# Kernel optimization log

Hardware: AMD Instinct MI355X
Metric: run time of the kernel (lower is better)

## Reference

```python
import jax, jax.numpy as jnp
import numpy as np

N_NODES = 100000
N_EDGES = 1600000
EMBED = 64


def setup_inputs() -> dict:
    key = jax.random.key(0)
    ks = jax.random.split(key, 8)
    scale = 1.0 / np.sqrt(EMBED)
    return {
        "embeddings": jax.random.normal(ks[0], (N_NODES, EMBED), dtype=jnp.float32),
        "edge_index": jax.random.randint(ks[1], (2, N_EDGES), 0, N_NODES, dtype=jnp.int32),
        "W1": jax.random.normal(ks[2], (EMBED, EMBED), dtype=jnp.float32) * scale,
        "b1": jnp.zeros((EMBED,), dtype=jnp.float32),
        "W2": jax.random.normal(ks[3], (EMBED, EMBED), dtype=jnp.float32) * scale,
        "b2": jnp.zeros((EMBED,), dtype=jnp.float32),
        "W3": jax.random.normal(ks[4], (EMBED, EMBED), dtype=jnp.float32) * scale,
        "b3": jnp.zeros((EMBED,), dtype=jnp.float32),
    }


def _gcn_layer(x, W, b, src, dst, n):
    # PyG GCNConv: add self-loops, symmetric normalization D^-1/2 (A+I) D^-1/2, then XW + b.
    x = x @ W  # [N, H]
    # degree from destination column, including the self-loop (+1)
    deg = jnp.zeros((n,), dtype=x.dtype).at[dst].add(1.0) + 1.0
    dinv = jax.lax.rsqrt(deg)  # deg >= 1, safe
    norm = dinv[src] * dinv[dst]  # [E]
    msg = x[src] * norm[:, None]  # [E, H] gather + scale
    out = jax.ops.segment_sum(msg, dst, num_segments=n)  # scatter-add
    out = out + x * (dinv * dinv)[:, None]  # self-loop term
    return out + b


def reference(embeddings, edge_index, W1, b1, W2, b2, W3, b3):
    src, dst = edge_index[0], edge_index[1]
    n = embeddings.shape[0]
    x = _gcn_layer(embeddings, W1, b1, src, dst, n)
    x = _gcn_layer(x, W2, b2, src, dst, n)
    x = _gcn_layer(x, W3, b3, src, dst, n)
    return x
```

## Files before the change

kernel.cpp:

```cpp
#include <hip/hip_runtime.h>

#define N_NODES 100000
#define N_EDGES 1600000
#define NTILES (N_NODES / 16)

#define BKT_SHIFT 8
#define BKT_NODES 256
#define NBK ((N_NODES + BKT_NODES - 1) / BKT_NODES)
#define CHUNK 4096
#define NCHUNKS ((N_EDGES + CHUNK - 1) / CHUNK)
#define BSTRIDE 5120

typedef _Float16 half8 __attribute__((ext_vector_type(8)));
typedef float floatx4 __attribute__((ext_vector_type(4)));

__device__ inline float h2f(unsigned short u) {
    return (float)__builtin_bit_cast(_Float16, u);
}
__device__ inline unsigned short f2h(float f) {
    return __builtin_bit_cast(unsigned short, (_Float16)f);
}

__global__ __launch_bounds__(512) void histA_kernel(const int* __restrict__ dst,
                                                    int* __restrict__ hist2d) {
    __shared__ int hist[NBK];
    int t = threadIdx.x;
    int e0 = blockIdx.x * CHUNK;
    int n = N_EDGES - e0; if (n > CHUNK) n = CHUNK;
    for (int i = t; i < NBK; i += 512) hist[i] = 0;
    __syncthreads();
    for (int i = t; i < n; i += 512) atomicAdd(&hist[dst[e0 + i] >> BKT_SHIFT], 1);
    __syncthreads();
    for (int i = t; i < NBK; i += 512) hist2d[blockIdx.x * NBK + i] = hist[i];
}

__global__ __launch_bounds__(512) void bscan_kernel(const int* __restrict__ hist2d,
                                                    int* __restrict__ base2d,
                                                    int* __restrict__ btot) {
    __shared__ int ss[512];
    int t = threadIdx.x;
    int b = blockIdx.x;
    int v = (t < NCHUNKS) ? hist2d[t * NBK + b] : 0;
    ss[t] = v;
    __syncthreads();
    for (int off = 1; off < 512; off <<= 1) {
        int u = (t >= off) ? ss[t - off] : 0;
        __syncthreads();
        ss[t] += u;
        __syncthreads();
    }
    if (t < NCHUNKS) base2d[t * NBK + b] = ss[t] - v;
    if (t == 511) btot[b] = ss[511];
}

__global__ __launch_bounds__(512) void binA3_kernel(const int* __restrict__ src,
                                                    const int* __restrict__ dst,
                                                    const int* __restrict__ base2d,
                                                    int* __restrict__ csr_tmp) {
    __shared__ int staged[CHUNK];
    __shared__ int delta[CHUNK];
    __shared__ int hist[NBK];
    __shared__ int lcur[NBK];
    __shared__ int gdel[NBK];
    __shared__ int scan_s[512];
    int t = threadIdx.x;
    int e0 = blockIdx.x * CHUNK;
    int n = N_EDGES - e0; if (n > CHUNK) n = CHUNK;

    for (int i = t; i < NBK; i += 512) hist[i] = 0;
    __syncthreads();
    for (int i = t; i < n; i += 512) atomicAdd(&hist[dst[e0 + i] >> BKT_SHIFT], 1);
    __syncthreads();
    int v = (t < NBK) ? hist[t] : 0;
    scan_s[t] = v;
    __syncthreads();
    for (int off = 1; off < 512; off <<= 1) {
        int u = (t >= off) ? scan_s[t - off] : 0;
        __syncthreads();
        scan_s[t] += u;
        __syncthreads();
    }
    if (t < NBK) {
        int excl = scan_s[t] - v;
        lcur[t] = excl;
        gdel[t] = t * BSTRIDE + base2d[blockIdx.x * NBK + t] - excl;
    }
    __syncthreads();
    for (int i = t; i < n; i += 512) {
        int s = src[e0 + i];
        int d = dst[e0 + i];
        int bkt = d >> BKT_SHIFT;
        int slot = atomicAdd(&lcur[bkt], 1);
        staged[slot] = ((d & 255) << 24) | s;
        delta[slot] = gdel[bkt];
    }
    __syncthreads();
    for (int p = t; p < n; p += 512) csr_tmp[delta[p] + p] = staged[p];
}

__global__ __launch_bounds__(512) void binB2_kernel(const int* __restrict__ btot,
                                                    const int* __restrict__ csr_tmp,
                                                    const float* __restrict__ emb,
                                                    int4* __restrict__ nodeinfo,
                                                    float* __restrict__ dinv,
                                                    int* __restrict__ csr,
                                                    unsigned short* __restrict__ Xs) {
    __shared__ int src_s[BSTRIDE];
    __shared__ unsigned char dloc[BSTRIDE];
    __shared__ int out_s[BSTRIDE];
    __shared__ int lcnt[BKT_NODES];
    __shared__ int ss[512];
    __shared__ int lcur[BKT_NODES];
    __shared__ float dinv_s[BKT_NODES];
    int t = threadIdx.x;
    int node0 = blockIdx.x * BKT_NODES;
    int base = blockIdx.x * BSTRIDE;
    int cnt = btot[blockIdx.x];
    if (cnt > BSTRIDE) cnt = BSTRIDE;
    if (t < BKT_NODES) lcnt[t] = 0;
    __syncthreads();
    for (int i = t; i < cnt; i += 512) {
        int e = csr_tmp[base + i];
        int dl = (unsigned int)e >> 24;
        src_s[i] = e & 0x00FFFFFF;
        dloc[i] = (unsigned char)dl;
        atomicAdd(&lcnt[dl], 1);
    }
    __syncthreads();
    int v = (t < BKT_NODES) ? lcnt[t] : 0;
    ss[t] = v;
    __syncthreads();
    for (int off = 1; off < 512; off <<= 1) {
        int u = (t >= off) ? ss[t - off] : 0;
        __syncthreads();
        ss[t] += u;
        __syncthreads();
    }
    int excl = ss[t] - v;
    int node = node0 + t;
    if (t < BKT_NODES) {
        lcur[t] = excl;
        if (node < N_NODES) {
            float dv = rsqrtf((float)v + 1.0f);
            nodeinfo[node] = make_int4(base + excl, v, __float_as_int(dv), 0);
            dinv[node] = dv;
            dinv_s[t] = dv;
        }
    }
    __syncthreads();
    for (int i = t; i < cnt; i += 512) {
        int slot = atomicAdd(&lcur[dloc[i]], 1);
        out_s[slot] = src_s[i];
    }
    __syncthreads();
    for (int i = t; i < cnt; i += 512) csr[base + i] = out_s[i];

    int nn = N_NODES - node0; if (nn > BKT_NODES) nn = BKT_NODES;
    const float4* E = (const float4*)emb;
    ushort4* X = (ushort4*)Xs;
    for (int f = t; f < nn * 16; f += 512) {
        int loc = f >> 4;
        float d = dinv_s[loc];
        float4 val = E[(size_t)(node0 + loc) * 16 + (f & 15)];
        ushort4 p;
        p.x = f2h(val.x * d); p.y = f2h(val.y * d);
        p.z = f2h(val.z * d); p.w = f2h(val.w * d);
        X[(size_t)(node0 + loc) * 16 + (f & 15)] = p;
    }
}

__global__ __launch_bounds__(256) void gather_kernel(
    const unsigned short* __restrict__ Xs,
    const int4* __restrict__ nodeinfo, const int* __restrict__ csr,
    unsigned short* __restrict__ Agg, int n_waves) {
    int lane = threadIdx.x & 63;
    int wid = (blockIdx.x * blockDim.x + threadIdx.x) >> 6;
    int sub = lane >> 4;
    int l16 = lane & 15;
    const ushort4* Xv = (const ushort4*)Xs;
    ushort4* Av = (ushort4*)Agg;

    for (int node = wid; node < N_NODES; node += n_waves) {
        int4 ni = nodeinfo[node];
        int beg = ni.x, end = ni.x + ni.y;
        float di = __int_as_float(ni.z);
        float4 acc = make_float4(0.f, 0.f, 0.f, 0.f);
        if (sub == 0) {
            ushort4 o = Xv[(size_t)node * 16 + l16];
            acc.x = h2f(o.x); acc.y = h2f(o.y); acc.z = h2f(o.z); acc.w = h2f(o.w);
        }
        int i = beg + sub;
        int sA0 = (i      < end) ? csr[i]      : 0;
        int sA1 = (i + 4  < end) ? csr[i + 4]  : 0;
        int sB0 = (i + 8  < end) ? csr[i + 8]  : 0;
        int sB1 = (i + 12 < end) ? csr[i + 12] : 0;
        ushort4 rA0 = Xv[(size_t)sA0 * 16 + l16];
        ushort4 rA1 = Xv[(size_t)sA1 * 16 + l16];
        while (i < end) {
            ushort4 rB0 = Xv[(size_t)sB0 * 16 + l16];
            ushort4 rB1 = Xv[(size_t)sB1 * 16 + l16];
            int sC0 = (i + 16 < end) ? csr[i + 16] : 0;
            int sC1 = (i + 20 < end) ? csr[i + 20] : 0;
            float m1 = (i + 4 < end) ? 1.0f : 0.0f;
            acc.x += h2f(rA0.x); acc.y += h2f(rA0.y);
            acc.z += h2f(rA0.z); acc.w += h2f(rA0.w);
            acc.x = fmaf(h2f(rA1.x), m1, acc.x);
            acc.y = fmaf(h2f(rA1.y), m1, acc.y);
            acc.z = fmaf(h2f(rA1.z), m1, acc.z);
            acc.w = fmaf(h2f(rA1.w), m1, acc.w);
            rA0 = rB0; rA1 = rB1;
            sB0 = sC0; sB1 = sC1;
            i += 8;
        }
        acc.x += __shfl_xor(acc.x, 16, 64); acc.y += __shfl_xor(acc.y, 16, 64);
        acc.z += __shfl_xor(acc.z, 16, 64); acc.w += __shfl_xor(acc.w, 16, 64);
        acc.x += __shfl_xor(acc.x, 32, 64); acc.y += __shfl_xor(acc.y, 32, 64);
        acc.z += __shfl_xor(acc.z, 32, 64); acc.w += __shfl_xor(acc.w, 32, 64);
        if (sub == 0) {
            ushort4 p;
            p.x = f2h(acc.x * di); p.y = f2h(acc.y * di);
            p.z = f2h(acc.z * di); p.w = f2h(acc.w * di);
            Av[(size_t)node * 16 + l16] = p;
        }
    }
}

__global__ __launch_bounds__(256) void mlp_mfma_kernel(
    const unsigned short* __restrict__ A, const float* __restrict__ W,
    const float* __restrict__ b, const float* __restrict__ dinv,
    unsigned short* __restrict__ out16, float* __restrict__ out32) {
    __shared__ __attribute__((aligned(16))) _Float16 Wh[4096];
    __shared__ __attribute__((aligned(16))) _Float16 Wl[4096];
    int tid = threadIdx.x;
    for (int u = tid; u < 4096; u += 256) {
        int kk = u >> 6, col = u & 63;
        int tt = col >> 4, mm = col & 15, cc = kk >> 5, gg = (kk >> 3) & 3, jj = kk & 7;
        float w = W[u];
        _Float16 h = (_Float16)w;
        int di = (tt * 2 + cc) * 512 + gg * 128 + mm * 8 + jj;
        Wh[di] = h;
        Wl[di] = (_Float16)(w - (float)h);
    }
    __syncthreads();

    int l = tid & 63;
    int wv = tid >> 6;
    int m = l & 15;
    int g = l >> 4;
    int tile = blockIdx.x * 4 + wv;
    if (tile >= NTILES) return;
    int node0 = tile * 16;
    int row = node0 + m;

    const half8* Ar = (const half8*)(A + (size_t)row * 64);
    half8 ah0 = Ar[g];
    half8 ah1 = Ar[4 + g];

    float bfrag[4];
#pragma unroll
    for (int t = 0; t < 4; t++) bfrag[t] = b[16 * t + m];
    float dv[4];
#pragma unroll
    for (int r = 0; r < 4; r++) dv[r] = dinv[node0 + 4 * g + r];

#pragma unroll
    for (int t = 0; t < 4; t++) {
        half8 bwh0 = *(const half8*)&Wh[(t * 2 + 0) * 512 + g * 128 + m * 8];
        half8 bwl0 = *(const half8*)&Wl[(t * 2 + 0) * 512 + g * 128 + m * 8];
        half8 bwh1 = *(const half8*)&Wh[(t * 2 + 1) * 512 + g * 128 + m * 8];
        half8 bwl1 = *(const half8*)&Wl[(t * 2 + 1) * 512 + g * 128 + m * 8];
        floatx4 d4 = {0.f, 0.f, 0.f, 0.f};
        d4 = __builtin_amdgcn_mfma_f32_16x16x32_f16(ah0, bwh0, d4, 0, 0, 0);
        d4 = __builtin_amdgcn_mfma_f32_16x16x32_f16(ah0, bwl0, d4, 0, 0, 0);
        d4 = __builtin_amdgcn_mfma_f32_16x16x32_f16(ah1, bwh1, d4, 0, 0, 0);
        d4 = __builtin_amdgcn_mfma_f32_16x16x32_f16(ah1, bwl1, d4, 0, 0, 0);
#pragma unroll
        for (int r = 0; r < 4; r++) {
            float v = d4[r] + bfrag[t];
            size_t idx = (size_t)(node0 + 4 * g + r) * 64 + 16 * t + m;
            if (out16) out16[idx] = f2h(v * dv[r]);
            else out32[idx] = v;
        }
    }
}

extern "C" void kernel_launch(void* const* d_in, const int* in_sizes, int n_in,
                              void* d_out, int out_size, void* d_ws, size_t ws_size,
                              hipStream_t stream) {
    const float* emb = (const float*)d_in[0];
    const int* edge  = (const int*)d_in[1];
    const float* W1 = (const float*)d_in[2];
    const float* b1 = (const float*)d_in[3];
    const float* W2 = (const float*)d_in[4];
    const float* b2 = (const float*)d_in[5];
    const float* W3 = (const float*)d_in[6];
    const float* b3 = (const float*)d_in[7];
    float* out = (float*)d_out;

    const int* src = edge;
    const int* dst = edge + N_EDGES;

    char* ws = (char*)d_ws;
    size_t off = 0;
    int* btot = (int*)(ws + off);        off += 2048;
    int* hist2d = (int*)(ws + off);      off += 612352;
    int* base2d = (int*)(ws + off);      off += 612352;
    int4* nodeinfo = (int4*)(ws + off);  off += 1600512;
    float* dinv = (float*)(ws + off);    off += 400128;
    int* csr_tmp = (int*)(ws + off);     off += 8007680;
    int* csr = (int*)(ws + off);         off += 8007680;
    unsigned short* Xa16 = (unsigned short*)(ws + off); off += 12800000;
    unsigned short* Xb16 = (unsigned short*)(ws + off); off += 12800000;
    unsigned short* Agg = (unsigned short*)(ws + off); off += 12800000;

    histA_kernel<<<NCHUNKS, 512, 0, stream>>>(dst, hist2d);
    bscan_kernel<<<NBK, 512, 0, stream>>>(hist2d, base2d, btot);
    binA3_kernel<<<NCHUNKS, 512, 0, stream>>>(src, dst, base2d, csr_tmp);
    binB2_kernel<<<NBK, 512, 0, stream>>>(btot, csr_tmp, emb, nodeinfo, dinv, csr, Xa16);

    const int GBLOCKS = 2048;
    const int n_waves = GBLOCKS * 256 / 64;
    const int MBLOCKS = (NTILES + 3) / 4;

    gather_kernel<<<GBLOCKS, 256, 0, stream>>>(Xa16, nodeinfo, csr, Agg, n_waves);
    mlp_mfma_kernel<<<MBLOCKS, 256, 0, stream>>>(Agg, W1, b1, dinv, Xb16, nullptr);
    gather_kernel<<<GBLOCKS, 256, 0, stream>>>(Xb16, nodeinfo, csr, Agg, n_waves);
    mlp_mfma_kernel<<<MBLOCKS, 256, 0, stream>>>(Agg, W2, b2, dinv, Xa16, nullptr);
    gather_kernel<<<GBLOCKS, 256, 0, stream>>>(Xa16, nodeinfo, csr, Agg, n_waves);
    mlp_mfma_kernel<<<MBLOCKS, 256, 0, stream>>>(Agg, W3, b3, dinv, nullptr, out);
}
```

Before: 267.6 us.

## Fold bucket scan into binning kernels and reuse precomputed chunk histograms

Removes the separate bucket-scan kernel. Each binning block now computes its own per-bucket global base by summing the histograms of all earlier chunks, and reads its local histogram from hist2d instead of recounting dst with shared atomics. binB2 gets its bucket total through a block reduction over the chunk histograms. This saves one launch and one pass over dst, but later blocks do O(NCHUNKS) strided reads of hist2d per bucket, which is redundant work spread across the grid.

```diff
diff --git a/kernel.cpp b/kernel.cpp
--- a/kernel.cpp
+++ b/kernel.cpp
@@ -34,32 +34,12 @@
     for (int i = t; i < NBK; i += 512) hist2d[blockIdx.x * NBK + i] = hist[i];
 }
 
-__global__ __launch_bounds__(512) void bscan_kernel(const int* __restrict__ hist2d,
-                                                    int* __restrict__ base2d,
-                                                    int* __restrict__ btot) {
-    __shared__ int ss[512];
-    int t = threadIdx.x;
-    int b = blockIdx.x;
-    int v = (t < NCHUNKS) ? hist2d[t * NBK + b] : 0;
-    ss[t] = v;
-    __syncthreads();
-    for (int off = 1; off < 512; off <<= 1) {
-        int u = (t >= off) ? ss[t - off] : 0;
-        __syncthreads();
-        ss[t] += u;
-        __syncthreads();
-    }
-    if (t < NCHUNKS) base2d[t * NBK + b] = ss[t] - v;
-    if (t == 511) btot[b] = ss[511];
-}
-
 __global__ __launch_bounds__(512) void binA3_kernel(const int* __restrict__ src,
                                                     const int* __restrict__ dst,
-                                                    const int* __restrict__ base2d,
+                                                    const int* __restrict__ hist2d,
                                                     int* __restrict__ csr_tmp) {
     __shared__ int staged[CHUNK];
     __shared__ int delta[CHUNK];
-    __shared__ int hist[NBK];
     __shared__ int lcur[NBK];
     __shared__ int gdel[NBK];
     __shared__ int scan_s[512];
@@ -67,11 +47,18 @@
     int e0 = blockIdx.x * CHUNK;
     int n = N_EDGES - e0; if (n > CHUNK) n = CHUNK;
 
-    for (int i = t; i < NBK; i += 512) hist[i] = 0;
-    __syncthreads();
-    for (int i = t; i < n; i += 512) atomicAdd(&hist[dst[e0 + i] >> BKT_SHIFT], 1);
-    __syncthreads();
-    int v = (t < NBK) ? hist[t] : 0;
+    int v = (t < NBK) ? hist2d[blockIdx.x * NBK + t] : 0;
+
+    int base_t = 0;
+    if (t < NBK) {
+        int lim = blockIdx.x, cc = 0;
+        for (; cc + 3 < lim; cc += 4) {
+            base_t += hist2d[(cc + 0) * NBK + t] + hist2d[(cc + 1) * NBK + t]
+                    + hist2d[(cc + 2) * NBK + t] + hist2d[(cc + 3) * NBK + t];
+        }
+        for (; cc < lim; cc++) base_t += hist2d[cc * NBK + t];
+    }
+
     scan_s[t] = v;
     __syncthreads();
     for (int off = 1; off < 512; off <<= 1) {
@@ -83,7 +70,7 @@
     if (t < NBK) {
         int excl = scan_s[t] - v;
         lcur[t] = excl;
-        gdel[t] = t * BSTRIDE + base2d[blockIdx.x * NBK + t] - excl;
+        gdel[t] = t * BSTRIDE + base_t - excl;
     }
     __syncthreads();
     for (int i = t; i < n; i += 512) {
@@ -98,7 +85,7 @@
     for (int p = t; p < n; p += 512) csr_tmp[delta[p] + p] = staged[p];
 }
 
-__global__ __launch_bounds__(512) void binB2_kernel(const int* __restrict__ btot,
+__global__ __launch_bounds__(512) void binB2_kernel(const int* __restrict__ hist2d,
                                                     const int* __restrict__ csr_tmp,
                                                     const float* __restrict__ emb,
                                                     int4* __restrict__ nodeinfo,
@@ -115,8 +102,19 @@
     int t = threadIdx.x;
     int node0 = blockIdx.x * BKT_NODES;
     int base = blockIdx.x * BSTRIDE;
-    int cnt = btot[blockIdx.x];
+
+    int part = 0;
+    for (int cc = t; cc < NCHUNKS; cc += 512) part += hist2d[cc * NBK + blockIdx.x];
+    ss[t] = part;
+    __syncthreads();
+    for (int off = 256; off > 0; off >>= 1) {
+        if (t < off) ss[t] += ss[t + off];
+        __syncthreads();
+    }
+    int cnt = ss[0];
     if (cnt > BSTRIDE) cnt = BSTRIDE;
+    __syncthreads();
+
     if (t < BKT_NODES) lcnt[t] = 0;
     __syncthreads();
     for (int i = t; i < cnt; i += 512) {
@@ -302,9 +300,7 @@
 
     char* ws = (char*)d_ws;
     size_t off = 0;
-    int* btot = (int*)(ws + off);        off += 2048;
     int* hist2d = (int*)(ws + off);      off += 612352;
-    int* base2d = (int*)(ws + off);      off += 612352;
     int4* nodeinfo = (int4*)(ws + off);  off += 1600512;
     float* dinv = (float*)(ws + off);    off += 400128;
     int* csr_tmp = (int*)(ws + off);     off += 8007680;
@@ -314,9 +310,8 @@
     unsigned short* Agg = (unsigned short*)(ws + off); off += 12800000;
 
     histA_kernel<<<NCHUNKS, 512, 0, stream>>>(dst, hist2d);
-    bscan_kernel<<<NBK, 512, 0, stream>>>(hist2d, base2d, btot);
-    binA3_kernel<<<NCHUNKS, 512, 0, stream>>>(src, dst, base2d, csr_tmp);
-    binB2_kernel<<<NBK, 512, 0, stream>>>(btot, csr_tmp, emb, nodeinfo, dinv, csr, Xa16);
+    binA3_kernel<<<NCHUNKS, 512, 0, stream>>>(src, dst, hist2d, csr_tmp);
+    binB2_kernel<<<NBK, 512, 0, stream>>>(hist2d, csr_tmp, emb, nodeinfo, dinv, csr, Xa16);
 
     const int GBLOCKS = 2048;
     const int n_waves = GBLOCKS * 256 / 64;
```

Measured after the change: 279.4 us. 1.04x slower.
